# Kernel tuning notes

Measured on AMD Instinct MI355X. Metric: run time of the kernel, lower is better.

Reference implementation:

```python
import jax, jax.numpy as jnp
import numpy as np

D = 128          # embed_features
N = 4096         # cells per batch
M = 8192         # genes / regions
FB1, FB2, FR, FA = 100, 100, 256, 512


def setup_inputs() -> dict:
    key = jax.random.key(0)
    ks = jax.random.split(key, 16)
    s = 0.05  # weight scale to keep activations in a sane range
    return {
        "u1": jax.random.normal(ks[0], (N, FB1), jnp.float32),
        "u2": jax.random.normal(ks[1], (N, FB2), jnp.float32),
        "v1": jax.random.normal(ks[2], (M, FR), jnp.float32),
        "v2": jax.random.normal(ks[3], (M, FA), jnp.float32),
        # linear layers stored as [in, out] so y = x @ W
        "Wb1": jax.random.normal(ks[4], (FB1, D), jnp.float32) * s,
        "Wb2": jax.random.normal(ks[5], (FB2, D), jnp.float32) * s,
        "Wrna1": jax.random.normal(ks[6], (FR, 2 * D), jnp.float32) * s,
        "Wrna2": jax.random.normal(ks[7], (2 * D, D), jnp.float32) * s,
        "gene_act": jax.random.normal(ks[8], (FA, FR), jnp.float32) * s,
        "w_prod1": jax.random.normal(ks[9], (D,), jnp.float32),
        "w_add1": jax.random.normal(ks[10], (2 * D,), jnp.float32),
        "w_prod2": jax.random.normal(ks[11], (D,), jnp.float32),
        "w_add2": jax.random.normal(ks[12], (2 * D,), jnp.float32),
        "bias_1": jax.random.normal(ks[13], (), jnp.float32),
        "bias_2": jax.random.normal(ks[14], (), jnp.float32),
    }


def _pair_scores(eu, ev, w_prod, w_add, bias):
    # Algebraically identical to the original all-pairs form:
    #   (eu[:,None,:] * ev[None,:,:]) @ w_prod  ==  (eu * w_prod) @ ev.T
    #   cat(eu, ev) @ w_add  ==  eu @ w_add[:D]  +  ev @ w_add[D:]
    prod = (eu * w_prod) @ ev.T                     # [N, M]
    add = (eu @ w_add[:D])[:, None] + (ev @ w_add[D:])[None, :]
    return prod + add + bias                        # [N, M]


def reference(u1, u2, v1, v2, Wb1, Wb2, Wrna1, Wrna2, gene_act,
              w_prod1, w_add1, w_prod2, w_add2, bias_1, bias_2):
    # mode='linear' activations -> identity
    embed_u1 = u1 @ Wb1                                          # [N, D]
    embed_v1 = jax.nn.relu(v1 @ Wrna1) @ Wrna2                   # [M, D]
    out1 = jax.nn.relu(_pair_scores(embed_u1, embed_v1, w_prod1, w_add1, bias_1))

    embed_u2 = u2 @ Wb2                                          # [N, D]
    embed_v2 = jax.nn.relu((v2 @ gene_act) @ Wrna1) @ Wrna2      # [M, D]
    out2 = jax.nn.sigmoid(_pair_scores(embed_u2, embed_v2, w_prod2, w_add2, bias_2))

    return out1, out2, embed_u1, embed_v1, embed_u2, embed_v2
```

## Files before the change

### kernel.cpp

```cpp
#include <hip/hip_runtime.h>
#include <math.h>

#define N_CELLS 4096
#define M_GENES 8192

typedef __attribute__((ext_vector_type(8))) short short8;
typedef __attribute__((ext_vector_type(4))) float f32x4;

__device__ __align__(16) float g_a[24576];

__device__ __align__(16) short g_bu1[N_CELLS * 128];
__device__ __align__(16) short g_bv1[M_GENES * 128];
__device__ __align__(16) short g_bu2[N_CELLS * 128];
__device__ __align__(16) short g_bv2[M_GENES * 128];

__device__ __align__(16) short g_gaT[256 * 512];
__device__ __align__(16) short g_W1T[256 * 256];
__device__ __align__(16) short g_W2T[128 * 256];


__device__ __forceinline__ short* bf_sel(int s) {
    switch (s) {
        case 0:  return g_bu1;
        case 1:  return g_bv1;
        case 2:  return g_bu2;
        default: return g_bv2;
    }
}

__device__ __forceinline__ const short* wt_sel(int s) {
    switch (s) {
        case 0:  return g_gaT;
        case 1:  return g_W1T;
        default: return g_W2T;
    }
}

__device__ __forceinline__ short f2bf(float f) {
    unsigned u = __builtin_bit_cast(unsigned, f);
    u += 0x7FFFu + ((u >> 16) & 1u);
    return (short)(u >> 16);
}

__device__ __forceinline__ void cvt8(const float* __restrict__ in, short* __restrict__ out) {
    const float4 x0 = *reinterpret_cast<const float4*>(in);
    const float4 x1 = *reinterpret_cast<const float4*>(in + 4);
    short8 o;
    o[0] = f2bf(x0.x); o[1] = f2bf(x0.y); o[2] = f2bf(x0.z); o[3] = f2bf(x0.w);
    o[4] = f2bf(x1.x); o[5] = f2bf(x1.y); o[6] = f2bf(x1.z); o[7] = f2bf(x1.w);
    *reinterpret_cast<short8*>(out) = o;
}

__device__ __forceinline__ void transpose8(const float* __restrict__ in, short* __restrict__ out,
                                           int c, int K, int Nc) {
    const int o0 = c * 8;
    const int ncol = o0 / K;
    const int k0 = o0 % K;
    short8 o;
#pragma unroll
    for (int j = 0; j < 8; ++j) o[j] = f2bf(in[(size_t)(k0 + j) * Nc + ncol]);
    *reinterpret_cast<short8*>(out + o0) = o;
}

__global__ __launch_bounds__(256) void prep_emb(const float* __restrict__ v1,
                                                const float* __restrict__ v2,
                                                const float* __restrict__ gene_act,
                                                const float* __restrict__ W1,
                                                const float* __restrict__ W2,
                                                short* __restrict__ cv1,
                                                short* __restrict__ cv2,
                                                const float* __restrict__ u1,
                                                const float* __restrict__ u2,
                                                const float* __restrict__ Wb1,
                                                const float* __restrict__ Wb2,
                                                const float* __restrict__ w_prod1,
                                                const float* __restrict__ w_add1,
                                                const float* __restrict__ w_prod2,
                                                const float* __restrict__ w_add2,
                                                float* __restrict__ eu1,
                                                float* __restrict__ eu2)
{
    __shared__ float sU[2][128];
    __shared__ float s2[4];
    const int b = blockIdx.x, t = threadIdx.x;
    if (b < 1024) {
        const int c = b * 256 + t;
        cvt8(v1 + (size_t)c * 8, cv1 + (size_t)c * 8);
    } else if (b < 3072) {
        const int c = (b - 1024) * 256 + t;
        cvt8(v2 + (size_t)c * 8, cv2 + (size_t)c * 8);
    } else if (b < 3136) {
        transpose8(gene_act, g_gaT, (b - 3072) * 256 + t, 512, 256);
    } else if (b < 3168) {
        transpose8(W1, g_W1T, (b - 3136) * 256 + t, 256, 256);
    } else if (b < 3184) {
        transpose8(W2, g_W2T, (b - 3168) * 256 + t, 256, 128);
    } else {
        const int which = (b < 5232) ? 0 : 1;
        const int bl = b - (which ? 5232 : 3184);
        const float* u      = which ? u2 : u1;
        const float* Wb     = which ? Wb2 : Wb1;
        const float* w_prod = which ? w_prod2 : w_prod1;
        const float* w_add  = which ? w_add2 : w_add1;
        float* e            = which ? eu2 : eu1;
        short* bu           = bf_sel(which ? 2 : 0);
        const int a_ofs     = which ? 12288 : 0;
        const int half = t >> 7;
        const int row = bl * 2 + half;
        const int d = t & 127;
        if (d < 100) sU[half][d] = u[row * 100 + d];
        __syncthreads();
        float acc = 0.f;
#pragma unroll
        for (int k = 0; k < 100; ++k) acc = fmaf(sU[half][k], Wb[k * 128 + d], acc);
        e[row * 128 + d] = acc;
        bu[row * 128 + d] = f2bf(acc * w_prod[d]);
        float v = acc * w_add[d];
#pragma unroll
        for (int off = 32; off > 0; off >>= 1) v += __shfl_down(v, off, 64);
        if ((t & 63) == 0) s2[t >> 6] = v;
        __syncthreads();
        if (t == 0)   g_a[a_ofs + row]     = s2[0] + s2[1];
        if (t == 128) g_a[a_ofs + row]     = s2[2] + s2[3];
    }
}

struct Job {
    const short* A;
    short* outb_ptr;
    float* outf;
    const float* w_addv;
    int bt_sel;
    int outb_sel;
    int a_ofs;
    int K;
    int relu;
    int nx;
};

__global__ __launch_bounds__(256) void chain2(Job j0, Job j1, int split)
{
    __shared__ __align__(16) short sA[128 * 128];
    __shared__ __align__(16) short sB[128 * 128];
    __shared__ float sRow[128];
    const int t = threadIdx.x;
    const int l = t & 63;
    int b = blockIdx.x;
    const Job j = (b < split) ? j0 : j1;
    if (b >= split) b -= split;
    const int bx = b & (j.nx - 1);
    const int by = (j.nx == 2) ? (b >> 1) : b;
    const int row0 = by * 128, col0 = bx * 128;
    const int K = j.K;
    const int Nc = j.nx * 128;
    const short* BT = wt_sel(j.bt_sel);
    short* outb = (j.outb_sel >= 0) ? bf_sel(j.outb_sel) : j.outb_ptr;

    const int w  = t >> 6;
    const int wm = (w >> 1) * 64;
    const int wn = (w & 1) * 64;
    const int lr  = l & 15;
    const int lkb = (l >> 4) * 16;

    f32x4 acc[4][4] = {};
    for (int k0 = 0; k0 < K; k0 += 128) {
        {
            const char* gA = (const char*)(j.A + (size_t)row0 * K + k0);
            const char* gB = (const char*)(BT + (size_t)col0 * K + k0);
            char* cA = (char*)sA;
            char* cB = (char*)sB;
#pragma unroll
            for (int c = 0; c < 8; ++c) {
                const int idx = c * 256 + t;
                const int row = idx >> 4;
                const int sub = idx & 15;
                const int dst = row * 256 + ((sub * 16) ^ ((row & 7) << 4));
                const size_t src = (size_t)row * (2 * K) + sub * 16;
                const short8 va = *reinterpret_cast<const short8*>(gA + src);
                const short8 vb = *reinterpret_cast<const short8*>(gB + src);
                *reinterpret_cast<short8*>(cA + dst) = va;
                *reinterpret_cast<short8*>(cB + dst) = vb;
            }
        }
        __syncthreads();
        const char* cA = (const char*)sA;
        const char* cB = (const char*)sB;
#pragma unroll
        for (int kk = 0; kk < 4; ++kk) {
            const int kb = kk * 64 + lkb;
            short8 a[4], bfr[4];
#pragma unroll
            for (int i = 0; i < 4; ++i) {
                const int rowA = wm + i * 16 + lr;
                a[i] = *reinterpret_cast<const short8*>(cA + rowA * 256 + (kb ^ ((rowA & 7) << 4)));
                const int rowB = wn + i * 16 + lr;
                bfr[i] = *reinterpret_cast<const short8*>(cB + rowB * 256 + (kb ^ ((rowB & 7) << 4)));
            }
#pragma unroll
            for (int i = 0; i < 4; ++i)
#pragma unroll
                for (int jj = 0; jj < 4; ++jj)
                    acc[i][jj] = __builtin_amdgcn_mfma_f32_16x16x32_bf16(a[i], bfr[jj], acc[i][jj], 0, 0, 0);
        }
        __syncthreads();
    }

    const int r4 = (l >> 4) * 4;
    const bool rd = (j.w_addv != nullptr);
    float wv[4];
    float part[4][4];
    if (rd) {
#pragma unroll
        for (int jj = 0; jj < 4; ++jj) wv[jj] = j.w_addv[wn + jj * 16 + lr];
#pragma unroll
        for (int i = 0; i < 4; ++i)
#pragma unroll
            for (int r = 0; r < 4; ++r) part[i][r] = 0.f;
    }
#pragma unroll
    for (int i = 0; i < 4; ++i) {
#pragma unroll
        for (int r = 0; r < 4; ++r) {
            const int grow = row0 + wm + i * 16 + r4 + r;
#pragma unroll
            for (int jj = 0; jj < 4; ++jj) {
                float x = acc[i][jj][r];
                if (j.relu) x = fmaxf(x, 0.f);
                const size_t oi = (size_t)grow * Nc + col0 + wn + jj * 16 + lr;
                outb[oi] = f2bf(x);
                if (j.outf) j.outf[oi] = x;
                if (rd) part[i][r] = fmaf(x, wv[jj], part[i][r]);
            }
        }
    }
    if (rd) {
#pragma unroll
        for (int off = 1; off < 16; off <<= 1)
#pragma unroll
            for (int i = 0; i < 4; ++i)
#pragma unroll
                for (int r = 0; r < 4; ++r)
                    part[i][r] += __shfl_xor(part[i][r], off, 64);
        if (t < 128) sRow[t] = 0.f;
        __syncthreads();
        if ((l & 15) == 0) {
#pragma unroll
            for (int i = 0; i < 4; ++i)
#pragma unroll
                for (int r = 0; r < 4; ++r)
                    atomicAdd(&sRow[wm + i * 16 + r4 + r], part[i][r]);
        }
        __syncthreads();
        if (t < 128) g_a[j.a_ofs + row0 + t] = sRow[t];
    }
}

__global__ __launch_bounds__(256) void pair_both(const float* __restrict__ bias1,
                                                 const float* __restrict__ bias2,
                                                 float* __restrict__ out1,
                                                 float* __restrict__ out2)
{
    __shared__ __align__(16) short sA[128 * 128];
    __shared__ __align__(16) short sB[128 * 128];
    const int which = blockIdx.z;
    const int t = threadIdx.x;
    const int l = t & 63;
    const int row0 = blockIdx.y * 128;
    const int col0 = blockIdx.x * 128;

    {
        const short8* gA = reinterpret_cast<const short8*>(bf_sel(which ? 2 : 0)) + (size_t)row0 * 16;
        const short8* gB = reinterpret_cast<const short8*>(bf_sel(which ? 3 : 1)) + (size_t)col0 * 16;
        char* cA = (char*)sA;
        char* cB = (char*)sB;
#pragma unroll
        for (int c = 0; c < 8; ++c) {
            const int idx = c * 256 + t;
            const int row = idx >> 4;
            const int sub = idx & 15;
            const int dst = row * 256 + ((sub * 16) ^ ((row & 7) << 4));
            const short8 va = gA[idx];
            const short8 vb = gB[idx];
            *reinterpret_cast<short8*>(cA + dst) = va;
            *reinterpret_cast<short8*>(cB + dst) = vb;
        }
    }
    __syncthreads();

    const int w  = t >> 6;
    const int wm = (w >> 1) * 64;
    const int wn = (w & 1) * 64;
    const int lr = l & 15;
    const int lkb = (l >> 4) * 16;

    f32x4 acc[4][4] = {};
    const char* cA = (const char*)sA;
    const char* cB = (const char*)sB;
#pragma unroll
    for (int kk = 0; kk < 4; ++kk) {
        const int kb = kk * 64 + lkb;
        short8 a[4], bfr[4];
#pragma unroll
        for (int i = 0; i < 4; ++i) {
            const int rowA = wm + i * 16 + lr;
            a[i] = *reinterpret_cast<const short8*>(cA + rowA * 256 + (kb ^ ((rowA & 7) << 4)));
            const int rowB = wn + i * 16 + lr;
            bfr[i] = *reinterpret_cast<const short8*>(cB + rowB * 256 + (kb ^ ((rowB & 7) << 4)));
        }
#pragma unroll
        for (int i = 0; i < 4; ++i)
#pragma unroll
            for (int jj = 0; jj < 4; ++jj)
                acc[i][jj] = __builtin_amdgcn_mfma_f32_16x16x32_bf16(a[i], bfr[jj], acc[i][jj], 0, 0, 0);
    }

    const float bias = which ? *bias2 : *bias1;
    float* outp = which ? out2 : out1;
    const int ofsU = which ? 12288 : 0;
    const int ofsV = which ? 16384 : 4096;
    const int r4 = (l >> 4) * 4;
    float au[4][4];
#pragma unroll
    for (int i = 0; i < 4; ++i)
#pragma unroll
        for (int r = 0; r < 4; ++r)
            au[i][r] = g_a[ofsU + row0 + wm + i * 16 + r4 + r];
    float av[4];
#pragma unroll
    for (int jj = 0; jj < 4; ++jj)
        av[jj] = g_a[ofsV + col0 + wn + jj * 16 + lr];

#pragma unroll
    for (int i = 0; i < 4; ++i) {
#pragma unroll
        for (int r = 0; r < 4; ++r) {
            const int grow = row0 + wm + i * 16 + r4 + r;
            float* orow = outp + (size_t)grow * M_GENES + col0 + wn;
#pragma unroll
            for (int jj = 0; jj < 4; ++jj) {
                float x = acc[i][jj][r] + au[i][r] + av[jj] + bias;
                if (which == 0) x = fmaxf(x, 0.f);
                else            x = __builtin_amdgcn_rcpf(1.f + __expf(-x));
                orow[jj * 16 + lr] = x;
            }
        }
    }
}

extern "C" void kernel_launch(void* const* d_in, const int* in_sizes, int n_in,
                              void* d_out, int out_size, void* d_ws, size_t ws_size,
                              hipStream_t stream)
{
    const float* u1       = (const float*)d_in[0];
    const float* u2       = (const float*)d_in[1];
    const float* v1       = (const float*)d_in[2];
    const float* v2       = (const float*)d_in[3];
    const float* Wb1      = (const float*)d_in[4];
    const float* Wb2      = (const float*)d_in[5];
    const float* Wrna1    = (const float*)d_in[6];
    const float* Wrna2    = (const float*)d_in[7];
    const float* gene_act = (const float*)d_in[8];
    const float* w_prod1  = (const float*)d_in[9];
    const float* w_add1   = (const float*)d_in[10];
    const float* w_prod2  = (const float*)d_in[11];
    const float* w_add2   = (const float*)d_in[12];
    const float* bias1    = (const float*)d_in[13];
    const float* bias2    = (const float*)d_in[14];

    float* out  = (float*)d_out;
    float* out1 = out;
    float* out2 = out1 + (size_t)N_CELLS * M_GENES;
    float* eu1  = out2 + (size_t)N_CELLS * M_GENES;
    float* ev1  = eu1 + N_CELLS * 128;
    float* eu2  = ev1 + M_GENES * 128;
    float* ev2  = eu2 + N_CELLS * 128;

    short* cv1 = (short*)out2;
    short* cv2 = cv1 + (size_t)M_GENES * 256;
    short* H0  = cv2 + (size_t)M_GENES * 512;
    short* H1  = H0  + (size_t)M_GENES * 256;
    short* H0b = H1  + (size_t)M_GENES * 256;

    prep_emb<<<7280, 256, 0, stream>>>(v1, v2, gene_act, Wrna1, Wrna2, cv1, cv2,
                                       u1, u2, Wb1, Wb2, w_prod1, w_add1,
                                       w_prod2, w_add2, eu1, eu2);

    Job jH1 = { cv2, H1, nullptr, nullptr, 0, -1, 0,     512, 0, 2 };
    Job jH0 = { cv1, H0, nullptr, nullptr, 1, -1, 0,     256, 1, 2 };
    chain2<<<256, 256, 0, stream>>>(jH1, jH0, 128);

    Job jev1 = { H0, nullptr, ev1, w_add1 + 128, 2, 1, 4096,  256, 0, 1 };
    Job jH0b = { H1, H0b, nullptr, nullptr,      1, -1, 0,    256, 1, 2 };
    chain2<<<192, 256, 0, stream>>>(jev1, jH0b, 64);

    Job jev2 = { H0b, nullptr, ev2, w_add2 + 128, 2, 3, 16384, 256, 0, 1 };
    chain2<<<64, 256, 0, stream>>>(jev2, jev2, 64);

    pair_both<<<dim3(64, 32, 2), 256, 0, stream>>>(bias1, bias2, out1, out2);
}
```

Baseline: 117.7 us.

## Fuse fp32-to-bf16 conversion into chain GEMMs and merge stages with embed/pair work

```diff
diff --git a/kernel.cpp b/kernel.cpp
--- a/kernel.cpp
+++ b/kernel.cpp
@@ -62,71 +62,9 @@
     *reinterpret_cast<short8*>(out + o0) = o;
 }
 
-__global__ __launch_bounds__(256) void prep_emb(const float* __restrict__ v1,
-                                                const float* __restrict__ v2,
-                                                const float* __restrict__ gene_act,
-                                                const float* __restrict__ W1,
-                                                const float* __restrict__ W2,
-                                                short* __restrict__ cv1,
-                                                short* __restrict__ cv2,
-                                                const float* __restrict__ u1,
-                                                const float* __restrict__ u2,
-                                                const float* __restrict__ Wb1,
-                                                const float* __restrict__ Wb2,
-                                                const float* __restrict__ w_prod1,
-                                                const float* __restrict__ w_add1,
-                                                const float* __restrict__ w_prod2,
-                                                const float* __restrict__ w_add2,
-                                                float* __restrict__ eu1,
-                                                float* __restrict__ eu2)
-{
-    __shared__ float sU[2][128];
-    __shared__ float s2[4];
-    const int b = blockIdx.x, t = threadIdx.x;
-    if (b < 1024) {
-        const int c = b * 256 + t;
-        cvt8(v1 + (size_t)c * 8, cv1 + (size_t)c * 8);
-    } else if (b < 3072) {
-        const int c = (b - 1024) * 256 + t;
-        cvt8(v2 + (size_t)c * 8, cv2 + (size_t)c * 8);
-    } else if (b < 3136) {
-        transpose8(gene_act, g_gaT, (b - 3072) * 256 + t, 512, 256);
-    } else if (b < 3168) {
-        transpose8(W1, g_W1T, (b - 3136) * 256 + t, 256, 256);
-    } else if (b < 3184) {
-        transpose8(W2, g_W2T, (b - 3168) * 256 + t, 256, 128);
-    } else {
-        const int which = (b < 5232) ? 0 : 1;
-        const int bl = b - (which ? 5232 : 3184);
-        const float* u      = which ? u2 : u1;
-        const float* Wb     = which ? Wb2 : Wb1;
-        const float* w_prod = which ? w_prod2 : w_prod1;
-        const float* w_add  = which ? w_add2 : w_add1;
-        float* e            = which ? eu2 : eu1;
-        short* bu           = bf_sel(which ? 2 : 0);
-        const int a_ofs     = which ? 12288 : 0;
-        const int half = t >> 7;
-        const int row = bl * 2 + half;
-        const int d = t & 127;
-        if (d < 100) sU[half][d] = u[row * 100 + d];
-        __syncthreads();
-        float acc = 0.f;
-#pragma unroll
-        for (int k = 0; k < 100; ++k) acc = fmaf(sU[half][k], Wb[k * 128 + d], acc);
-        e[row * 128 + d] = acc;
-        bu[row * 128 + d] = f2bf(acc * w_prod[d]);
-        float v = acc * w_add[d];
-#pragma unroll
-        for (int off = 32; off > 0; off >>= 1) v += __shfl_down(v, off, 64);
-        if ((t & 63) == 0) s2[t >> 6] = v;
-        __syncthreads();
-        if (t == 0)   g_a[a_ofs + row]     = s2[0] + s2[1];
-        if (t == 128) g_a[a_ofs + row]     = s2[2] + s2[3];
-    }
-}
-
 struct Job {
     const short* A;
+    const float* Af;
     short* outb_ptr;
     float* outf;
     const float* w_addv;
@@ -138,66 +76,69 @@
     int nx;
 };
 
-__global__ __launch_bounds__(256) void chain2(Job j0, Job j1, int split)
-{
-    __shared__ __align__(16) short sA[128 * 128];
-    __shared__ __align__(16) short sB[128 * 128];
-    __shared__ float sRow[128];
-    const int t = threadIdx.x;
-    const int l = t & 63;
-    int b = blockIdx.x;
-    const Job j = (b < split) ? j0 : j1;
-    if (b >= split) b -= split;
-    const int bx = b & (j.nx - 1);
+__device__ __forceinline__ void chain_block(const Job& j, int b,
+                                            short* sAs, short* sBs, float* sRow)
+{
+    const int t = threadIdx.x, l = t & 63;
+    const int bx = (j.nx == 2) ? (b & 1) : 0;
     const int by = (j.nx == 2) ? (b >> 1) : b;
-    const int row0 = by * 128, col0 = bx * 128;
-    const int K = j.K;
-    const int Nc = j.nx * 128;
+    const int row0 = by * 64, col0 = bx * 128;
+    const int K = j.K, Nc = j.nx * 128;
     const short* BT = wt_sel(j.bt_sel);
     short* outb = (j.outb_sel >= 0) ? bf_sel(j.outb_sel) : j.outb_ptr;
-
-    const int w  = t >> 6;
-    const int wm = (w >> 1) * 64;
-    const int wn = (w & 1) * 64;
-    const int lr  = l & 15;
-    const int lkb = (l >> 4) * 16;
-
-    f32x4 acc[4][4] = {};
+    const int w = t >> 6, wm = (w >> 1) * 32, wn = (w & 1) * 64;
+    const int lr = l & 15, lkb = (l >> 4) * 16;
+    char* cA = (char*)sAs;
+    char* cB = (char*)sBs;
+
+    f32x4 acc[2][4] = {};
     for (int k0 = 0; k0 < K; k0 += 128) {
+        if (j.Af) {
+            const float* gAf = j.Af + (size_t)row0 * K + k0;
+#pragma unroll
+            for (int c = 0; c < 4; ++c) {
+                const int idx = c * 256 + t;
+                const int row = idx >> 4, sub = idx & 15;
+                const int dst = row * 256 + ((sub * 16) ^ ((row & 7) << 4));
+                cvt8(gAf + (size_t)row * K + sub * 8, (short*)(cA + dst));
+            }
+        } else {
+            const char* gA = (const char*)(j.A + (size_t)row0 * K + k0);
+#pragma unroll
+            for (int c = 0; c < 4; ++c) {
+                const int idx = c * 256 + t;
+                const int row = idx >> 4, sub = idx & 15;
+                const int dst = row * 256 + ((sub * 16) ^ ((row & 7) << 4));
+                *(short8*)(cA + dst) = *(const short8*)(gA + (size_t)row * (2 * K) + sub * 16);
+            }
+        }
         {
-            const char* gA = (const char*)(j.A + (size_t)row0 * K + k0);
             const char* gB = (const char*)(BT + (size_t)col0 * K + k0);
-            char* cA = (char*)sA;
-            char* cB = (char*)sB;
 #pragma unroll
             for (int c = 0; c < 8; ++c) {
                 const int idx = c * 256 + t;
-                const int row = idx >> 4;
-                const int sub = idx & 15;
+                const int row = idx >> 4, sub = idx & 15;
                 const int dst = row * 256 + ((sub * 16) ^ ((row & 7) << 4));
-                const size_t src = (size_t)row * (2 * K) + sub * 16;
-                const short8 va = *reinterpret_cast<const short8*>(gA + src);
-                const short8 vb = *reinterpret_cast<const short8*>(gB + src);
-                *reinterpret_cast<short8*>(cA + dst) = va;
-                *reinterpret_cast<short8*>(cB + dst) = vb;
+                *(short8*)(cB + dst) = *(const short8*)(gB + (size_t)row * (2 * K) + sub * 16);
             }
         }
         __syncthreads();
-        const char* cA = (const char*)sA;
-        const char* cB = (const char*)sB;
 #pragma unroll
         for (int kk = 0; kk < 4; ++kk) {
             const int kb = kk * 64 + lkb;
-            short8 a[4], bfr[4];
-#pragma unroll
-            for (int i = 0; i < 4; ++i) {
+            short8 a[2], bfr[4];
+#pragma unroll
+            for (int i = 0; i < 2; ++i) {
                 const int rowA = wm + i * 16 + lr;
-                a[i] = *reinterpret_cast<const short8*>(cA + rowA * 256 + (kb ^ ((rowA & 7) << 4)));
-                const int rowB = wn + i * 16 + lr;
-                bfr[i] = *reinterpret_cast<const short8*>(cB + rowB * 256 + (kb ^ ((rowB & 7) << 4)));
-            }
-#pragma unroll
-            for (int i = 0; i < 4; ++i)
+                a[i] = *(const short8*)(cA + rowA * 256 + (kb ^ ((rowA & 7) << 4)));
+            }
+#pragma unroll
+            for (int jj = 0; jj < 4; ++jj) {
+                const int rowB = wn + jj * 16 + lr;
+                bfr[jj] = *(const short8*)(cB + rowB * 256 + (kb ^ ((rowB & 7) << 4)));
+            }
+#pragma unroll
+            for (int i = 0; i < 2; ++i)
 #pragma unroll
                 for (int jj = 0; jj < 4; ++jj)
                     acc[i][jj] = __builtin_amdgcn_mfma_f32_16x16x32_bf16(a[i], bfr[jj], acc[i][jj], 0, 0, 0);
@@ -207,18 +148,17 @@
 
     const int r4 = (l >> 4) * 4;
     const bool rd = (j.w_addv != nullptr);
-    float wv[4];
-    float part[4][4];
+    float wv[4], part[2][4];
     if (rd) {
 #pragma unroll
         for (int jj = 0; jj < 4; ++jj) wv[jj] = j.w_addv[wn + jj * 16 + lr];
 #pragma unroll
-        for (int i = 0; i < 4; ++i)
+        for (int i = 0; i < 2; ++i)
 #pragma unroll
             for (int r = 0; r < 4; ++r) part[i][r] = 0.f;
     }
 #pragma unroll
-    for (int i = 0; i < 4; ++i) {
+    for (int i = 0; i < 2; ++i) {
 #pragma unroll
         for (int r = 0; r < 4; ++r) {
             const int grow = row0 + wm + i * 16 + r4 + r;
@@ -237,52 +177,45 @@
 #pragma unroll
         for (int off = 1; off < 16; off <<= 1)
 #pragma unroll
-            for (int i = 0; i < 4; ++i)
+            for (int i = 0; i < 2; ++i)
 #pragma unroll
                 for (int r = 0; r < 4; ++r)
                     part[i][r] += __shfl_xor(part[i][r], off, 64);
-        if (t < 128) sRow[t] = 0.f;
+        if (t < 64) sRow[t] = 0.f;
         __syncthreads();
         if ((l & 15) == 0) {
 #pragma unroll
-            for (int i = 0; i < 4; ++i)
+            for (int i = 0; i < 2; ++i)
 #pragma unroll
                 for (int r = 0; r < 4; ++r)
                     atomicAdd(&sRow[wm + i * 16 + r4 + r], part[i][r]);
         }
         __syncthreads();
-        if (t < 128) g_a[j.a_ofs + row0 + t] = sRow[t];
-    }
-}
-
-__global__ __launch_bounds__(256) void pair_both(const float* __restrict__ bias1,
-                                                 const float* __restrict__ bias2,
-                                                 float* __restrict__ out1,
-                                                 float* __restrict__ out2)
-{
-    __shared__ __align__(16) short sA[128 * 128];
-    __shared__ __align__(16) short sB[128 * 128];
-    const int which = blockIdx.z;
-    const int t = threadIdx.x;
-    const int l = t & 63;
-    const int row0 = blockIdx.y * 128;
-    const int col0 = blockIdx.x * 128;
-
+        if (t < 64) g_a[j.a_ofs + row0 + t] = sRow[t];
+    }
+}
+
+__device__ __forceinline__ void pair_block(int which, int bb, short* sAs, short* sBs,
+                                           const float* bias1, const float* bias2,
+                                           float* out1, float* out2)
+{
+    const int t = threadIdx.x, l = t & 63;
+    const int col0 = (bb & 63) * 128;
+    const int row0 = (bb >> 6) * 128;
+    char* cA = (char*)sAs;
+    char* cB = (char*)sBs;
     {
         const short8* gA = reinterpret_cast<const short8*>(bf_sel(which ? 2 : 0)) + (size_t)row0 * 16;
         const short8* gB = reinterpret_cast<const short8*>(bf_sel(which ? 3 : 1)) + (size_t)col0 * 16;
-        char* cA = (char*)sA;
-        char* cB = (char*)sB;
 #pragma unroll
         for (int c = 0; c < 8; ++c) {
             const int idx = c * 256 + t;
-            const int row = idx >> 4;
-            const int sub = idx & 15;
+            const int row = idx >> 4, sub = idx & 15;
             const int dst = row * 256 + ((sub * 16) ^ ((row & 7) << 4));
             const short8 va = gA[idx];
             const short8 vb = gB[idx];
-            *reinterpret_cast<short8*>(cA + dst) = va;
-            *reinterpret_cast<short8*>(cB + dst) = vb;
+            *(short8*)(cA + dst) = va;
+            *(short8*)(cB + dst) = vb;
         }
     }
     __syncthreads();
@@ -294,8 +227,6 @@
     const int lkb = (l >> 4) * 16;
 
     f32x4 acc[4][4] = {};
-    const char* cA = (const char*)sA;
-    const char* cB = (const char*)sB;
 #pragma unroll
     for (int kk = 0; kk < 4; ++kk) {
         const int kb = kk * 64 + lkb;
@@ -303,9 +234,9 @@
 #pragma unroll
         for (int i = 0; i < 4; ++i) {
             const int rowA = wm + i * 16 + lr;
-            a[i] = *reinterpret_cast<const short8*>(cA + rowA * 256 + (kb ^ ((rowA & 7) << 4)));
+            a[i] = *(const short8*)(cA + rowA * 256 + (kb ^ ((rowA & 7) << 4)));
             const int rowB = wn + i * 16 + lr;
-            bfr[i] = *reinterpret_cast<const short8*>(cB + rowB * 256 + (kb ^ ((rowB & 7) << 4)));
+            bfr[i] = *(const short8*)(cB + rowB * 256 + (kb ^ ((rowB & 7) << 4)));
         }
 #pragma unroll
         for (int i = 0; i < 4; ++i)
@@ -345,6 +276,78 @@
             }
         }
     }
+}
+
+__device__ __forceinline__ void embed_block(int b,
+        const float* u1, const float* u2, const float* Wb1, const float* Wb2,
+        const float* wp1, const float* wa1, const float* wp2, const float* wa2,
+        float* eu1, float* eu2, float* sF)
+{
+    float* sU = sF;
+    float* s2 = sF + 256;
+    const int t = threadIdx.x;
+    const int which = (b >= 2048) ? 1 : 0;
+    const int bl = which ? (b - 2048) : b;
+    const float* u      = which ? u2 : u1;
+    const float* Wb     = which ? Wb2 : Wb1;
+    const float* w_prod = which ? wp2 : wp1;
+    const float* w_add  = which ? wa2 : wa1;
+    float* e            = which ? eu2 : eu1;
+    short* bu           = bf_sel(which ? 2 : 0);
+    const int a_ofs     = which ? 12288 : 0;
+    const int half = t >> 7;
+    const int row = bl * 2 + half;
+    const int d = t & 127;
+    if (d < 100) sU[half * 128 + d] = u[row * 100 + d];
+    __syncthreads();
+    float acc = 0.f;
+#pragma unroll
+    for (int k = 0; k < 100; ++k) acc = fmaf(sU[half * 128 + k], Wb[k * 128 + d], acc);
+    e[row * 128 + d] = acc;
+    bu[row * 128 + d] = f2bf(acc * w_prod[d]);
+    float v = acc * w_add[d];
+#pragma unroll
+    for (int off = 32; off > 0; off >>= 1) v += __shfl_down(v, off, 64);
+    if ((t & 63) == 0) s2[t >> 6] = v;
+    __syncthreads();
+    if (t == 0)   g_a[a_ofs + row] = s2[0] + s2[1];
+    if (t == 128) g_a[a_ofs + row] = s2[2] + s2[3];
+}
+
+__global__ __launch_bounds__(256) void prep_w(const float* __restrict__ gene_act,
+                                              const float* __restrict__ W1,
+                                              const float* __restrict__ W2)
+{
+    const int b = blockIdx.x, t = threadIdx.x;
+    if (b < 64)      transpose8(gene_act, g_gaT, b * 256 + t, 512, 256);
+    else if (b < 96) transpose8(W1, g_W1T, (b - 64) * 256 + t, 256, 256);
+    else             transpose8(W2, g_W2T, (b - 96) * 256 + t, 256, 128);
+}
+
+__global__ __launch_bounds__(256) void chain_embed(Job j0, Job j1, int split, int nchain,
+        const float* u1, const float* u2, const float* Wb1, const float* Wb2,
+        const float* wp1, const float* wa1, const float* wp2, const float* wa2,
+        float* eu1, float* eu2)
+{
+    __shared__ __align__(16) short sMem[24576];
+    __shared__ float sF[264];
+    const int b = blockIdx.x;
+    if (b < nchain) {
+        if (b < split) chain_block(j0, b, sMem, sMem + 8192, sF);
+        else           chain_block(j1, b - split, sMem, sMem + 8192, sF);
+    } else {
+        embed_block(b - nchain, u1, u2, Wb1, Wb2, wp1, wa1, wp2, wa2, eu1, eu2, sF);
+    }
+}
+
+__global__ __launch_bounds__(256) void pair_chain(Job j, int nchain, int which,
+        const float* bias1, const float* bias2, float* out1, float* out2)
+{
+    __shared__ __align__(16) short sMem[32768];
+    __shared__ float sF[264];
+    const int b = blockIdx.x;
+    if (b < nchain) chain_block(j, b, sMem, sMem + 8192, sF);
+    else            pair_block(which, b - nchain, sMem, sMem + 16384, bias1, bias2, out1, out2);
 }
 
 extern "C" void kernel_launch(void* const* d_in, const int* in_sizes, int n_in,
@@ -375,26 +378,25 @@
     float* eu2  = ev1 + M_GENES * 128;
     float* ev2  = eu2 + N_CELLS * 128;
 
-    short* cv1 = (short*)out2;
-    short* cv2 = cv1 + (size_t)M_GENES * 256;
-    short* H0  = cv2 + (size_t)M_GENES * 512;
-    short* H1  = H0  + (size_t)M_GENES * 256;
-    short* H0b = H1  + (size_t)M_GENES * 256;
-
-    prep_emb<<<7280, 256, 0, stream>>>(v1, v2, gene_act, Wrna1, Wrna2, cv1, cv2,
-                                       u1, u2, Wb1, Wb2, w_prod1, w_add1,
-                                       w_prod2, w_add2, eu1, eu2);
-
-    Job jH1 = { cv2, H1, nullptr, nullptr, 0, -1, 0,     512, 0, 2 };
-    Job jH0 = { cv1, H0, nullptr, nullptr, 1, -1, 0,     256, 1, 2 };
-    chain2<<<256, 256, 0, stream>>>(jH1, jH0, 128);
-
-    Job jev1 = { H0, nullptr, ev1, w_add1 + 128, 2, 1, 4096,  256, 0, 1 };
-    Job jH0b = { H1, H0b, nullptr, nullptr,      1, -1, 0,    256, 1, 2 };
-    chain2<<<192, 256, 0, stream>>>(jev1, jH0b, 64);
-
-    Job jev2 = { H0b, nullptr, ev2, w_add2 + 128, 2, 3, 16384, 256, 0, 1 };
-    chain2<<<64, 256, 0, stream>>>(jev2, jev2, 64);
-
-    pair_both<<<dim3(64, 32, 2), 256, 0, stream>>>(bias1, bias2, out1, out2);
-}
+    short* H0  = (short*)out2;
+    short* H1  = H0 + (size_t)M_GENES * 256;
+    short* H0b = H1 + (size_t)M_GENES * 256;
+
+    prep_w<<<112, 256, 0, stream>>>(gene_act, Wrna1, Wrna2);
+
+    Job jH1 = { nullptr, v2, H1, nullptr, nullptr, 0, -1, 0,     512, 0, 2 };
+    Job jH0 = { nullptr, v1, H0, nullptr, nullptr, 1, -1, 0,     256, 1, 2 };
+    chain_embed<<<4608, 256, 0, stream>>>(jH1, jH0, 256, 512,
+        u1, u2, Wb1, Wb2, w_prod1, w_add1, w_prod2, w_add2, eu1, eu2);
+
+    Job jev1 = { H0, nullptr, nullptr, ev1, w_add1 + 128, 2, 1, 4096,  256, 0, 1 };
+    Job jH0b = { H1, nullptr, H0b, nullptr, nullptr,      1, -1, 0,    256, 1, 2 };
+    chain_embed<<<384, 256, 0, stream>>>(jev1, jH0b, 128, 384,
+        u1, u2, Wb1, Wb2, w_prod1, w_add1, w_prod2, w_add2, eu1, eu2);
+
+    Job jev2 = { H0b, nullptr, nullptr, ev2, w_add2 + 128, 2, 3, 16384, 256, 0, 1 };
+    pair_chain<<<2176, 256, 0, stream>>>(jev2, 128, 0, bias1, bias2, out1, out2);
+
+    Job jnull = {};
+    pair_chain<<<2048, 256, 0, stream>>>(jnull, 0, 1, bias1, bias2, out1, out2);
+}
```

Result: faster. 112.1 us (-4.8%).
